# Kernel tuning notes

Measured on AMD Instinct MI355X. Metric: run time of the kernel, lower is better.

## Reference

```python
import jax, jax.numpy as jnp
import numpy as np

C = 64            # x_channel (d_model)
D = 2 * C         # d_inner (expand=2)
N = C // 2        # d_state
K = 4             # scan directions
R = -(-C // 16)   # dt_rank = ceil(d_model/16)
Bsz, H, W = 2, 48, 48
EPS = 1e-5


def setup_inputs() -> dict:
    key = jax.random.key(0)
    ks = jax.random.split(key, 8)
    g = lambda k, shp, s: jax.random.normal(k, shp, dtype=jnp.float32) * s
    return {
        "fufea1": g(ks[0], (Bsz, C, H, W), 1.0),
        "ln_g": jnp.ones((C,), jnp.float32),
        "ln_b": jnp.zeros((C,), jnp.float32),
        "in_proj_w": g(ks[1], (2 * D, C), C ** -0.5),
        "conv_w": g(ks[2], (D, 1, 3, 3), 1.0 / 3.0),   # depthwise 3x3
        "conv_b": g(ks[3], (D,), 0.02),
        "x_proj_w": g(ks[4], (K, R + 2 * N, D), D ** -0.5),
        "dt_w": g(ks[5], (K, D, R), R ** -0.5),
        "dt_b": g(ks[6], (K, D), 0.1),
        "A_logs": jnp.log(jnp.tile(jnp.arange(1, N + 1, dtype=jnp.float32), (K, D, 1))),  # S4D-real init
        "Ds": jnp.ones((K, D), jnp.float32),
        "out_ln_g": jnp.ones((D,), jnp.float32),
        "out_ln_b": jnp.zeros((D,), jnp.float32),
        "out_proj_w": g(ks[7], (C, D), D ** -0.5),
    }


def _layernorm(x, g, b):
    mu = x.mean(-1, keepdims=True)
    var = ((x - mu) ** 2).mean(-1, keepdims=True)
    return (x - mu) * jax.lax.rsqrt(var + EPS) * g + b


def reference(fufea1, ln_g, ln_b, in_proj_w, conv_w, conv_b, x_proj_w,
              dt_w, dt_b, A_logs, Ds, out_ln_g, out_ln_b, out_proj_w):
    B, Cc, Hh, Ww = fufea1.shape
    L = Hh * Ww
    # pre-LN (over channels, channels-last)
    xn = _layernorm(fufea1.transpose(0, 2, 3, 1), ln_g, ln_b)          # (B,H,W,C)
    # SS2D: in_proj -> split x,z
    xz = xn @ in_proj_w.T                                               # (B,H,W,2D)
    x, z = jnp.split(xz, 2, axis=-1)
    x = x.transpose(0, 3, 1, 2)                                         # (B,D,H,W)
    x = jax.lax.conv_general_dilated(x, conv_w, (1, 1), "SAME",
                                     feature_group_count=D,
                                     dimension_numbers=("NCHW", "OIHW", "NCHW"))
    x = jax.nn.silu(x + conv_b[None, :, None, None])
    # 4-direction sequences: row-major, col-major, and their reverses
    x_hw = x.reshape(B, D, L)
    x_wh = x.transpose(0, 1, 3, 2).reshape(B, D, L)
    xs = jnp.stack([x_hw, x_wh], axis=1)                                # (B,2,D,L)
    xs = jnp.concatenate([xs, jnp.flip(xs, axis=-1)], axis=1)           # (B,K,D,L)
    # per-direction projections of dt, B, C
    x_dbl = jnp.einsum("bkdl,kcd->bkcl", xs, x_proj_w)
    dts, Bs, Cs = jnp.split(x_dbl, [R, R + N], axis=2)                  # (B,K,R,L),(B,K,N,L),(B,K,N,L)
    dts = jnp.einsum("bkrl,kdr->bkdl", dts, dt_w)
    delta = jax.nn.softplus(dts + dt_b[None, :, :, None])               # (B,K,D,L)
    A = -jnp.exp(A_logs)                                                # (K,D,N)
    # selective scan over L; carry h: (B,K,D,N)
    u_l = xs.transpose(3, 0, 1, 2)                                      # (L,B,K,D)
    dt_l = delta.transpose(3, 0, 1, 2)
    B_l = Bs.transpose(3, 0, 1, 2)                                      # (L,B,K,N)
    C_l = Cs.transpose(3, 0, 1, 2)

    def step(h, inp):
        u_t, d_t, b_t, c_t = inp
        dA = jnp.exp(d_t[..., None] * A)                                # (B,K,D,N)
        h = dA * h + (d_t * u_t)[..., None] * b_t[:, :, None, :]
        y = jnp.einsum("bkdn,bkn->bkd", h, c_t)
        return h, y

    h0 = jnp.zeros((B, K, D, N), xs.dtype)
    _, ys = jax.lax.scan(step, h0, (u_l, dt_l, B_l, C_l))               # ys: (L,B,K,D)
    out_y = ys.transpose(1, 2, 3, 0) + Ds[None, :, :, None] * xs        # (B,K,D,L)
    # merge the 4 directions back to row-major hw order
    inv_y = jnp.flip(out_y[:, 2:4], axis=-1)                            # (B,2,D,L)
    wh = lambda t: t.reshape(B, D, Ww, Hh).transpose(0, 1, 3, 2).reshape(B, D, L)
    y = out_y[:, 0] + inv_y[:, 0] + wh(out_y[:, 1]) + wh(inv_y[:, 1])   # (B,D,L)
    y = y.transpose(0, 2, 1).reshape(B, Hh, Ww, D)
    y = _layernorm(y, out_ln_g, out_ln_b) * jax.nn.silu(z)
    out = (y @ out_proj_w.T).transpose(0, 3, 1, 2) + fufea1             # residual add
    return out
```

## Files before the change

### kernel.cpp

```cpp
#include <hip/hip_runtime.h>

#define Cc 64
#define Dd 128
#define Nn 32
#define Kk 4
#define Rr 4
#define Bb 2
#define Hh 48
#define Ww 48
#define Ll 2304
#define EPSf 1e-5f
#define LCc 144

#if __has_builtin(__builtin_amdgcn_exp2f)
#define EXP2F __builtin_amdgcn_exp2f
#else
#define EXP2F exp2f
#endif

__device__ __forceinline__ float wsum64(float v) {
  v += __shfl_xor(v, 32);
  v += __shfl_xor(v, 16);
  v += __shfl_xor(v, 8);
  v += __shfl_xor(v, 4);
  v += __shfl_xor(v, 2);
  v += __shfl_xor(v, 1);
  return v;
}

__device__ __forceinline__ float hmax32(float v) {
  v = fmaxf(v, __shfl_xor(v, 1));
  v = fmaxf(v, __shfl_xor(v, 2));
  v = fmaxf(v, __shfl_xor(v, 4));
  v = fmaxf(v, __shfl_xor(v, 8));
  v = fmaxf(v, __shfl_xor(v, 16));
  return v;
}

__device__ __forceinline__ int pixbase(int j, int k) {
  if (k == 0) return j;
  if (k == 2) return Ll - 1 - j;
  if (k == 1) return (j % Hh) * Ww + (j / Hh);
  const int jr = Ll - 1 - j;
  return (jr % Hh) * Ww + (jr / Hh);
}

__global__ __launch_bounds__(256) void k1_ln_inproj(
    const float* __restrict__ x, const float* __restrict__ g,
    const float* __restrict__ bta, const float* __restrict__ Wp,
    float* __restrict__ xin, float* __restrict__ zb)
{
  __shared__ float xS[16][65];
  __shared__ float xnS[16][64];
  const int tid = threadIdx.x;
  const int wv = tid >> 6, lane = tid & 63;
  const int pbase = blockIdx.x * 16;
  const int b = pbase / Ll;
  const int lbase = pbase % Ll;
  {
    const int c = tid >> 2, li0 = (tid & 3) * 4;
    const float4 v4 = *(const float4*)&x[(b * Cc + c) * Ll + lbase + li0];
    xS[li0 + 0][c] = v4.x;
    xS[li0 + 1][c] = v4.y;
    xS[li0 + 2][c] = v4.z;
    xS[li0 + 3][c] = v4.w;
  }
  __syncthreads();
  const float gv = g[lane], bv = bta[lane];
  for (int pi = 0; pi < 4; ++pi) {
    const int p = wv * 4 + pi;
    const float v = xS[p][lane];
    const float mu = wsum64(v) * (1.0f / 64.0f);
    const float dv = v - mu;
    const float var = wsum64(dv * dv) * (1.0f / 64.0f);
    const float rs = rsqrtf(var + EPSf);
    xnS[p][lane] = dv * rs * gv + bv;
  }
  __syncthreads();
  float acc[4][4];
  #pragma unroll
  for (int pi = 0; pi < 4; ++pi)
    #pragma unroll
    for (int m = 0; m < 4; ++m) acc[pi][m] = 0.f;
  const float4* W4 = (const float4*)Wp;
  #pragma unroll 4
  for (int c4 = 0; c4 < 16; ++c4) {
    float4 xn4[4];
    #pragma unroll
    for (int pi = 0; pi < 4; ++pi)
      xn4[pi] = ((const float4*)xnS[wv * 4 + pi])[c4];
    #pragma unroll
    for (int m = 0; m < 4; ++m) {
      const float4 w4 = W4[(lane + 64 * m) * 16 + c4];
      #pragma unroll
      for (int pi = 0; pi < 4; ++pi)
        acc[pi][m] += xn4[pi].x * w4.x + xn4[pi].y * w4.y +
                      xn4[pi].z * w4.z + xn4[pi].w * w4.w;
    }
  }
  #pragma unroll
  for (int pi = 0; pi < 4; ++pi) {
    const int l = lbase + wv * 4 + pi;
    const size_t base = (size_t)(b * Ll + l) * Dd;
    xin[base + lane]      = acc[pi][0];
    xin[base + lane + 64] = acc[pi][1];
    zb[base + lane]       = acc[pi][2];
    zb[base + lane + 64]  = acc[pi][3];
  }
}

__global__ __launch_bounds__(512) void k3_proj(
    const float* __restrict__ xin, const float* __restrict__ cw,
    const float* __restrict__ cb, const float* __restrict__ xpw,
    const float* __restrict__ dtw, const float* __restrict__ dtb,
    float* __restrict__ xc, float2* __restrict__ dd2,
    float* __restrict__ Bm, float* __restrict__ Cm)
{
  __shared__ float xinS[128][31];
  __shared__ float xvS[8][132];
  __shared__ float dtsS[8][16];
  const int t = threadIdx.x;
  const int pb = blockIdx.x * 8;
  const int b = pb / Ll;
  const int lb = pb % Ll;
  const int h0 = lb / Ww, w0 = lb % Ww;
  for (int i = t; i < 3840; i += 512) {
    const int d = i & 127, j = i >> 7;
    const int r = j / 10, c = j % 10;
    const int hh = h0 + r - 1, ww = w0 + c - 1;
    float v = 0.f;
    if (hh >= 0 && hh < Hh && ww >= 0 && ww < Ww)
      v = xin[((size_t)(b * Ll) + hh * Ww + ww) * Dd + d];
    xinS[d][j] = v;
  }
  __syncthreads();
  for (int i = t; i < 1024; i += 512) {
    const int pi = i >> 7, d = i & 127;
    float acc = cb[d];
    #pragma unroll
    for (int r = 0; r < 3; ++r)
      #pragma unroll
      for (int c = 0; c < 3; ++c)
        acc += xinS[d][r * 10 + pi + c] * cw[d * 9 + r * 3 + c];
    const float sig = 1.0f / (1.0f + __expf(-acc));
    xvS[pi][d] = acc * sig;
  }
  __syncthreads();
  if (t < 272) {
    const int k = t / 68, c = t % 68;
    const size_t bkL = (size_t)(b * Kk + k) * Ll;
    float acc[8];
    #pragma unroll
    for (int pi = 0; pi < 8; ++pi) acc[pi] = 0.f;
    const float4* w4p = (const float4*)(xpw + (k * 68 + c) * 128);
    for (int d4 = 0; d4 < 32; ++d4) {
      const float4 w4 = w4p[d4];
      #pragma unroll
      for (int pi = 0; pi < 8; ++pi) {
        const float4 x4 = ((const float4*)xvS[pi])[d4];
        acc[pi] += x4.x * w4.x + x4.y * w4.y + x4.z * w4.z + x4.w * w4.w;
      }
    }
    #pragma unroll
    for (int pi = 0; pi < 8; ++pi) {
      const int l0 = lb + pi;
      const int h = l0 / Ww, w = l0 % Ww;
      int lk;
      if      (k == 0) lk = l0;
      else if (k == 1) lk = w * Hh + h;
      else if (k == 2) lk = Ll - 1 - l0;
      else             lk = Ll - 1 - (w * Hh + h);
      if (c < Rr)            dtsS[pi][k * 4 + c] = acc[pi];
      else if (c < Rr + Nn)  Bm[(bkL + lk) * Nn + (c - Rr)] = acc[pi];
      else                   Cm[(bkL + lk) * Nn + (c - Rr - Nn)] = acc[pi];
    }
  } else {
    for (int i = t - 272; i < 1024; i += 240) {
      const int pi = i >> 7, d = i & 127;
      xc[((size_t)(b * Ll) + lb + pi) * Dd + d] = xvS[pi][d];
    }
  }
  __syncthreads();
  {
    const int k = t >> 7, dd = t & 127;
    const float4 dw = *(const float4*)&dtw[(k * Dd + dd) * 4];
    const float biasv = dtb[k * Dd + dd];
    float2* drow = dd2 + ((size_t)((b * Kk + k) * Dd) + dd) * Ll;
    float2 buf[8];
    #pragma unroll
    for (int pi = 0; pi < 8; ++pi) {
      const float a = biasv
          + dtsS[pi][k * 4 + 0] * dw.x + dtsS[pi][k * 4 + 1] * dw.y
          + dtsS[pi][k * 4 + 2] * dw.z + dtsS[pi][k * 4 + 3] * dw.w;
      const float sp = (a > 20.f) ? a : log1pf(__expf(a));
      buf[pi] = make_float2(sp, sp * xvS[pi][dd]);
    }
    float4* f4 = (float4*)(drow + lb);
    #pragma unroll
    for (int j = 0; j < 4; ++j)
      f4[j] = make_float4(buf[2 * j].x, buf[2 * j].y, buf[2 * j + 1].x, buf[2 * j + 1].y);
  }
}

__global__ __launch_bounds__(512) void k4_scan(
    const float2* __restrict__ dd2, const float* __restrict__ Bm,
    const float* __restrict__ Cm, const float* __restrict__ Alogs,
    float* __restrict__ ys)
{
  __shared__ float2 ddS[Ll];
  __shared__ float hendS[16][32];
  __shared__ float carryS[16][32];
  __shared__ float sumDS[16];
  __shared__ float cmaxS[16];
  __shared__ float pS[16][8][36];
  const int tid = threadIdx.x;
  const int s = tid >> 5, n = tid & 31;
  const int blk = blockIdx.x;
  const int bk = blk & 7;
  const int d = blk >> 3;
  const int b = bk >> 2, k = bk & 3;
  const float An = -__expf(Alogs[(k * Dd + d) * Nn + n]);
  const float AnE = An * 1.44269504f;
  const size_t bkL = (size_t)(b * Kk + k) * Ll;
  const float2* dP = dd2 + ((size_t)((b * Kk + k) * Dd) + d) * Ll;
  const float* bP = Bm + bkL * Nn + n;
  const float* cP = Cm + bkL * Nn + n;
  const int lbeg = s * LCc;
  float* yD = ys + ((size_t)((b * Kk + k) * Dd) + d) * Ll;
  const int pstr = (k == 0) ? 1 : (k == 1) ? Ww : (k == 2) ? -1 : -Ww;
  const int rrow = n & 7, qtr = n >> 3;

  {
    const float4* src = (const float4*)dP;
    float4* dst = (float4*)ddS;
    #pragma unroll
    for (int i = 0; i < 3; ++i) {
      const int idx = tid + i * 512;
      if (idx < Ll / 2) dst[idx] = src[idx];
    }
  }
  __syncthreads();

  float h = 0.f, sumD = 0.f, cmx = 0.f;
  {
    const float* bl = bP + (size_t)lbeg * Nn;
    const float* cl = cP + (size_t)lbeg * Nn;
    float b0 = bl[0], b1 = bl[Nn], b2 = bl[2 * Nn], b3 = bl[3 * Nn];
    float c0 = cl[0], c1 = cl[Nn], c2 = cl[2 * Nn], c3 = cl[3 * Nn];
    int pb = pixbase(lbeg, k);
    float2 q0 = ddS[pb], q1 = ddS[pb + pstr], q2 = ddS[pb + 2 * pstr], q3 = ddS[pb + 3 * pstr];
    for (int t8 = 0; t8 < LCc / 8; ++t8) {
      const int j0n = lbeg + t8 * 8 + 8;
      const int pbn = pixbase(j0n <= Ll - 8 ? j0n : Ll - 8, k);
      #pragma unroll
      for (int half = 0; half < 2; ++half) {
        bl += 4 * Nn; cl += 4 * Nn;
        const int gb = (half == 0) ? pb + 4 * pstr : pbn;
        const float2 qn0 = ddS[gb], qn1 = ddS[gb + pstr],
                     qn2 = ddS[gb + 2 * pstr], qn3 = ddS[gb + 3 * pstr];
        const float b0n = bl[0], b1n = bl[Nn], b2n = bl[2 * Nn], b3n = bl[3 * Nn];
        const float c0n = cl[0], c1n = cl[Nn], c2n = cl[2 * Nn], c3n = cl[3 * Nn];
        h = EXP2F(q0.x * AnE) * h + q0.y * b0; pS[s][half * 4 + 0][n] = h * c0;
        h = EXP2F(q1.x * AnE) * h + q1.y * b1; pS[s][half * 4 + 1][n] = h * c1;
        h = EXP2F(q2.x * AnE) * h + q2.y * b2; pS[s][half * 4 + 2][n] = h * c2;
        h = EXP2F(q3.x * AnE) * h + q3.y * b3; pS[s][half * 4 + 3][n] = h * c3;
        sumD += (q0.x + q1.x) + (q2.x + q3.x);
        cmx = fmaxf(cmx, fmaxf(fmaxf(fabsf(c0), fabsf(c1)),
                               fmaxf(fabsf(c2), fabsf(c3))));
        q0 = qn0; q1 = qn1; q2 = qn2; q3 = qn3;
        b0 = b0n; b1 = b1n; b2 = b2n; b3 = b3n;
        c0 = c0n; c1 = c1n; c2 = c2n; c3 = c3n;
      }
      const float4 a4 = *(const float4*)&pS[s][rrow][qtr * 8];
      const float4 d4v = *(const float4*)&pS[s][rrow][qtr * 8 + 4];
      float sum = ((a4.x + a4.y) + (a4.z + a4.w)) + ((d4v.x + d4v.y) + (d4v.z + d4v.w));
      sum += __shfl_xor(sum, 8);
      sum += __shfl_xor(sum, 16);
      if (n < 8) yD[pb + n * pstr] = sum;
      pb = pbn;
    }
  }
  hendS[s][n] = h;
  const float cmxAll = hmax32(cmx);
  if (n == 0) { sumDS[s] = sumD; cmaxS[s] = cmxAll; }
  __syncthreads();
  if (tid < 32) {
    float carry = 0.f;
    #pragma unroll
    for (int s2 = 0; s2 < 16; ++s2) {
      carryS[s2][tid] = carry;
      carry = EXP2F(AnE * sumDS[s2]) * carry + hendS[s2][tid];
    }
  }
  __syncthreads();
  const float carry = carryS[s][n];
  const float mc = hmax32(fabsf(carry));
  const float AmaxE = hmax32(AnE);
  const float Pstop = log2f(mc * cmaxS[s] * 3.2e6f) / (-AmaxE);
  {
    float hc = carry, P = 0.f;
    const float* cl = cP + (size_t)lbeg * Nn;
    for (int t8 = 0; t8 < LCc / 8; ++t8) {
      if (!(P < Pstop)) break;
      const int pb = pixbase(lbeg + t8 * 8, k);
      #pragma unroll
      for (int half = 0; half < 2; ++half) {
        const int gb = pb + half * 4 * pstr;
        const float2 qq0 = ddS[gb], qq1 = ddS[gb + pstr],
                     qq2 = ddS[gb + 2 * pstr], qq3 = ddS[gb + 3 * pstr];
        hc *= EXP2F(qq0.x * AnE); pS[s][half * 4 + 0][n] = hc * cl[0];
        hc *= EXP2F(qq1.x * AnE); pS[s][half * 4 + 1][n] = hc * cl[Nn];
        hc *= EXP2F(qq2.x * AnE); pS[s][half * 4 + 2][n] = hc * cl[2 * Nn];
        hc *= EXP2F(qq3.x * AnE); pS[s][half * 4 + 3][n] = hc * cl[3 * Nn];
        P += (qq0.x + qq1.x) + (qq2.x + qq3.x);
        cl += 4 * Nn;
      }
      const float4 a4 = *(const float4*)&pS[s][rrow][qtr * 8];
      const float4 d4v = *(const float4*)&pS[s][rrow][qtr * 8 + 4];
      float sum = ((a4.x + a4.y) + (a4.z + a4.w)) + ((d4v.x + d4v.y) + (d4v.z + d4v.w));
      sum += __shfl_xor(sum, 8);
      sum += __shfl_xor(sum, 16);
      if (n < 8) yD[pb + n * pstr] += sum;
    }
  }
}

__global__ __launch_bounds__(256) void k5_merge(
    const float* __restrict__ ys, const float* __restrict__ zb,
    const float* __restrict__ og, const float* __restrict__ ob,
    const float* __restrict__ Wo, const float* __restrict__ resid,
    const float* __restrict__ xc, const float* __restrict__ DsP,
    float* __restrict__ out)
{
  __shared__ float ysS[4][16][132];
  __shared__ float xcS[16][128];
  __shared__ float tS[16][128];
  __shared__ float oS[64][17];
  const int tid = threadIdx.x;
  const int wv = tid >> 6, lane = tid & 63;
  const int pbase = blockIdx.x * 16;
  const int b = pbase / Ll;
  const int lbase = pbase % Ll;
  {
    const int li0 = (tid & 3) * 4, dh = tid >> 2;
    #pragma unroll
    for (int it = 0; it < 2; ++it) {
      const int d = dh + 64 * it;
      #pragma unroll
      for (int k = 0; k < 4; ++k) {
        const float4 v = *(const float4*)&ys[((size_t)(b * Kk + k) * Dd + d) * Ll + lbase + li0];
        ysS[k][li0 + 0][d] = v.x; ysS[k][li0 + 1][d] = v.y;
        ysS[k][li0 + 2][d] = v.z; ysS[k][li0 + 3][d] = v.w;
      }
    }
  }
  {
    const int p = tid >> 4, q = tid & 15;
    const float4* src = (const float4*)&xc[((size_t)(b * Ll) + lbase + p) * Dd];
    ((float4*)xcS[p])[q]      = src[q];
    ((float4*)xcS[p])[q + 16] = src[q + 16];
  }
  float sDs[2];
  #pragma unroll
  for (int m = 0; m < 2; ++m) {
    const int dch = lane + 64 * m;
    sDs[m] = DsP[dch] + DsP[Dd + dch] + DsP[2 * Dd + dch] + DsP[3 * Dd + dch];
  }
  __syncthreads();
  for (int pi = 0; pi < 4; ++pi) {
    const int p = wv * 4 + pi;
    const int l0 = lbase + p;
    float tv[2];
    #pragma unroll
    for (int m = 0; m < 2; ++m) {
      const int dch = lane + 64 * m;
      tv[m] = ysS[0][p][dch] + ysS[1][p][dch] + ysS[2][p][dch] + ysS[3][p][dch]
            + sDs[m] * xcS[p][dch];
    }
    const float mu = wsum64(tv[0] + tv[1]) * (1.0f / 128.0f);
    const float q = wsum64((tv[0] - mu) * (tv[0] - mu) +
                           (tv[1] - mu) * (tv[1] - mu)) * (1.0f / 128.0f);
    const float rs = rsqrtf(q + EPSf);
    #pragma unroll
    for (int m = 0; m < 2; ++m) {
      const int dch = lane + 64 * m;
      const float zz = zb[(size_t)(b * Ll + l0) * Dd + dch];
      const float sig = 1.0f / (1.0f + __expf(-zz));
      tS[p][dch] = ((tv[m] - mu) * rs * og[dch] + ob[dch]) * (zz * sig);
    }
  }
  __syncthreads();
  float acc[4] = {0.f, 0.f, 0.f, 0.f};
  const float4* W4 = (const float4*)Wo;
  for (int d4 = 0; d4 < 32; ++d4) {
    const float4 w4 = W4[lane * 32 + d4];
    #pragma unroll
    for (int pi = 0; pi < 4; ++pi) {
      const float4 t4 = ((const float4*)tS[wv * 4 + pi])[d4];
      acc[pi] += t4.x * w4.x + t4.y * w4.y + t4.z * w4.z + t4.w * w4.w;
    }
  }
  #pragma unroll
  for (int pi = 0; pi < 4; ++pi) oS[lane][wv * 4 + pi] = acc[pi];
  __syncthreads();
  const int c = tid >> 2, off = (tid & 3) * 4;
  const size_t obase = (size_t)(b * Cc + c) * Ll + lbase + off;
  const float4 r4 = *(const float4*)(resid + obase);
  float4 o4;
  o4.x = oS[c][off + 0] + r4.x;
  o4.y = oS[c][off + 1] + r4.y;
  o4.z = oS[c][off + 2] + r4.z;
  o4.w = oS[c][off + 3] + r4.w;
  *(float4*)(out + obase) = o4;
}

extern "C" void kernel_launch(void* const* d_in, const int* in_sizes, int n_in,
                              void* d_out, int out_size, void* d_ws, size_t ws_size,
                              hipStream_t stream)
{
  (void)in_sizes; (void)n_in; (void)out_size; (void)ws_size;
  const float* fufea1     = (const float*)d_in[0];
  const float* ln_g       = (const float*)d_in[1];
  const float* ln_b       = (const float*)d_in[2];
  const float* in_proj_w  = (const float*)d_in[3];
  const float* conv_w     = (const float*)d_in[4];
  const float* conv_b     = (const float*)d_in[5];
  const float* x_proj_w   = (const float*)d_in[6];
  const float* dt_w       = (const float*)d_in[7];
  const float* dt_b       = (const float*)d_in[8];
  const float* A_logs     = (const float*)d_in[9];
  const float* Ds         = (const float*)d_in[10];
  const float* out_ln_g   = (const float*)d_in[11];
  const float* out_ln_b   = (const float*)d_in[12];
  const float* out_proj_w = (const float*)d_in[13];

  float* ws = (float*)d_ws;
  float2* dd2 = (float2*)ws;
  float* Bm   = ws + 4718592;
  float* Cm   = ws + 5308416;
  float* zb   = ws + 5898240;
  float* xc   = ws + 6488064;
  float* ysb  = ws + 7077888;
  float* xin  = ws + 7077888;

  k1_ln_inproj<<<288, 256, 0, stream>>>(fufea1, ln_g, ln_b, in_proj_w, xin, zb);
  k3_proj<<<576, 512, 0, stream>>>(xin, conv_w, conv_b, x_proj_w, dt_w, dt_b,
                                   xc, dd2, Bm, Cm);
  k4_scan<<<1024, 512, 0, stream>>>(dd2, Bm, Cm, A_logs, ysb);
  k5_merge<<<288, 256, 0, stream>>>(ysb, zb, out_ln_g, out_ln_b, out_proj_w, fufea1,
                                    xc, Ds, (float*)d_out);
}
```

Baseline: 187.0 us.

## Vectorize conv halo loads and reduce scan partial sums per 4-step half

In the projection kernel, the conv input tile changes from channel-major to pixel-major shared layout, so the halo loads become float4 global reads and float4 shared stores instead of scalar strided writes. In the scan kernel, the per-step h*C products are reduced across the state dimension after every 4 steps rather than every 8. This halves the pS scratch buffer. The trade is one extra shuffle stage per reduction and twice as many reduction rounds and output writes, in exchange for smaller shared memory and a shorter dependency window before each reduction.

Result: slower. 197.7 us (+5.7%).

```diff
diff --git a/kernel.cpp b/kernel.cpp
--- a/kernel.cpp
+++ b/kernel.cpp
@@ -116,7 +116,7 @@
     float* __restrict__ xc, float2* __restrict__ dd2,
     float* __restrict__ Bm, float* __restrict__ Cm)
 {
-  __shared__ float xinS[128][31];
+  __shared__ float xinS[30][128];
   __shared__ float xvS[8][132];
   __shared__ float dtsS[8][16];
   const int t = threadIdx.x;
@@ -124,14 +124,14 @@
   const int b = pb / Ll;
   const int lb = pb % Ll;
   const int h0 = lb / Ww, w0 = lb % Ww;
-  for (int i = t; i < 3840; i += 512) {
-    const int d = i & 127, j = i >> 7;
+  for (int i = t; i < 960; i += 512) {
+    const int j = i >> 5, d4 = i & 31;
     const int r = j / 10, c = j % 10;
     const int hh = h0 + r - 1, ww = w0 + c - 1;
-    float v = 0.f;
+    float4 v = make_float4(0.f, 0.f, 0.f, 0.f);
     if (hh >= 0 && hh < Hh && ww >= 0 && ww < Ww)
-      v = xin[((size_t)(b * Ll) + hh * Ww + ww) * Dd + d];
-    xinS[d][j] = v;
+      v = *(const float4*)&xin[((size_t)(b * Ll) + hh * Ww + ww) * Dd + d4 * 4];
+    *(float4*)&xinS[j][d4 * 4] = v;
   }
   __syncthreads();
   for (int i = t; i < 1024; i += 512) {
@@ -141,7 +141,7 @@
     for (int r = 0; r < 3; ++r)
       #pragma unroll
       for (int c = 0; c < 3; ++c)
-        acc += xinS[d][r * 10 + pi + c] * cw[d * 9 + r * 3 + c];
+        acc += xinS[r * 10 + pi + c][d] * cw[d * 9 + r * 3 + c];
     const float sig = 1.0f / (1.0f + __expf(-acc));
     xvS[pi][d] = acc * sig;
   }
@@ -212,7 +212,7 @@
   __shared__ float carryS[16][32];
   __shared__ float sumDS[16];
   __shared__ float cmaxS[16];
-  __shared__ float pS[16][8][36];
+  __shared__ float pS[16][4][36];
   const int tid = threadIdx.x;
   const int s = tid >> 5, n = tid & 31;
   const int blk = blockIdx.x;
@@ -228,7 +228,7 @@
   const int lbeg = s * LCc;
   float* yD = ys + ((size_t)((b * Kk + k) * Dd) + d) * Ll;
   const int pstr = (k == 0) ? 1 : (k == 1) ? Ww : (k == 2) ? -1 : -Ww;
-  const int rrow = n & 7, qtr = n >> 3;
+  const int rrow = n & 3, qtr = n >> 2;
 
   {
     const float4* src = (const float4*)dP;
@@ -260,23 +260,23 @@
                      qn2 = ddS[gb + 2 * pstr], qn3 = ddS[gb + 3 * pstr];
         const float b0n = bl[0], b1n = bl[Nn], b2n = bl[2 * Nn], b3n = bl[3 * Nn];
         const float c0n = cl[0], c1n = cl[Nn], c2n = cl[2 * Nn], c3n = cl[3 * Nn];
-        h = EXP2F(q0.x * AnE) * h + q0.y * b0; pS[s][half * 4 + 0][n] = h * c0;
-        h = EXP2F(q1.x * AnE) * h + q1.y * b1; pS[s][half * 4 + 1][n] = h * c1;
-        h = EXP2F(q2.x * AnE) * h + q2.y * b2; pS[s][half * 4 + 2][n] = h * c2;
-        h = EXP2F(q3.x * AnE) * h + q3.y * b3; pS[s][half * 4 + 3][n] = h * c3;
+        h = EXP2F(q0.x * AnE) * h + q0.y * b0; pS[s][0][n] = h * c0;
+        h = EXP2F(q1.x * AnE) * h + q1.y * b1; pS[s][1][n] = h * c1;
+        h = EXP2F(q2.x * AnE) * h + q2.y * b2; pS[s][2][n] = h * c2;
+        h = EXP2F(q3.x * AnE) * h + q3.y * b3; pS[s][3][n] = h * c3;
         sumD += (q0.x + q1.x) + (q2.x + q3.x);
         cmx = fmaxf(cmx, fmaxf(fmaxf(fabsf(c0), fabsf(c1)),
                                fmaxf(fabsf(c2), fabsf(c3))));
         q0 = qn0; q1 = qn1; q2 = qn2; q3 = qn3;
         b0 = b0n; b1 = b1n; b2 = b2n; b3 = b3n;
         c0 = c0n; c1 = c1n; c2 = c2n; c3 = c3n;
+        const float4 a4 = *(const float4*)&pS[s][rrow][qtr * 4];
+        float sum = (a4.x + a4.y) + (a4.z + a4.w);
+        sum += __shfl_xor(sum, 4);
+        sum += __shfl_xor(sum, 8);
+        sum += __shfl_xor(sum, 16);
+        if (n < 4) yD[pb + (half * 4 + n) * pstr] = sum;
       }
-      const float4 a4 = *(const float4*)&pS[s][rrow][qtr * 8];
-      const float4 d4v = *(const float4*)&pS[s][rrow][qtr * 8 + 4];
-      float sum = ((a4.x + a4.y) + (a4.z + a4.w)) + ((d4v.x + d4v.y) + (d4v.z + d4v.w));
-      sum += __shfl_xor(sum, 8);
-      sum += __shfl_xor(sum, 16);
-      if (n < 8) yD[pb + n * pstr] = sum;
       pb = pbn;
     }
   }
@@ -308,19 +308,19 @@
         const int gb = pb + half * 4 * pstr;
         const float2 qq0 = ddS[gb], qq1 = ddS[gb + pstr],
                      qq2 = ddS[gb + 2 * pstr], qq3 = ddS[gb + 3 * pstr];
-        hc *= EXP2F(qq0.x * AnE); pS[s][half * 4 + 0][n] = hc * cl[0];
-        hc *= EXP2F(qq1.x * AnE); pS[s][half * 4 + 1][n] = hc * cl[Nn];
-        hc *= EXP2F(qq2.x * AnE); pS[s][half * 4 + 2][n] = hc * cl[2 * Nn];
-        hc *= EXP2F(qq3.x * AnE); pS[s][half * 4 + 3][n] = hc * cl[3 * Nn];
+        hc *= EXP2F(qq0.x * AnE); pS[s][0][n] = hc * cl[0];
+        hc *= EXP2F(qq1.x * AnE); pS[s][1][n] = hc * cl[Nn];
+        hc *= EXP2F(qq2.x * AnE); pS[s][2][n] = hc * cl[2 * Nn];
+        hc *= EXP2F(qq3.x * AnE); pS[s][3][n] = hc * cl[3 * Nn];
         P += (qq0.x + qq1.x) + (qq2.x + qq3.x);
         cl += 4 * Nn;
+        const float4 a4 = *(const float4*)&pS[s][rrow][qtr * 4];
+        float sum = (a4.x + a4.y) + (a4.z + a4.w);
+        sum += __shfl_xor(sum, 4);
+        sum += __shfl_xor(sum, 8);
+        sum += __shfl_xor(sum, 16);
+        if (n < 4) yD[pb + (half * 4 + n) * pstr] += sum;
       }
-      const float4 a4 = *(const float4*)&pS[s][rrow][qtr * 8];
-      const float4 d4v = *(const float4*)&pS[s][rrow][qtr * 8 + 4];
-      float sum = ((a4.x + a4.y) + (a4.z + a4.w)) + ((d4v.x + d4v.y) + (d4v.z + d4v.w));
-      sum += __shfl_xor(sum, 8);
-      sum += __shfl_xor(sum, 16);
-      if (n < 8) yD[pb + n * pstr] += sum;
     }
   }
 }
```
